# Kernel tuning notes

Hardware: AMD Instinct MI355X
Metric: run time of the kernel (lower is better)

Reference implementation:

```python
import jax, jax.numpy as jnp
import numpy as np

N_NODES = 50000


def gcn_conv(x, W, b, src, dst, n_nodes):
    # GCNConv (PyG defaults): h = x @ W; symmetric normalization with self-loops;
    # out[i] = sum_{(j->i) in E} d_j^-1/2 d_i^-1/2 h[j] + d_i^-1 h[i] + b
    h = x @ W
    ones = jnp.ones(src.shape[0], dtype=x.dtype)
    deg = jax.ops.segment_sum(ones, dst, num_segments=n_nodes) + 1.0  # +1 self-loop
    dinv = jax.lax.rsqrt(deg)
    norm = dinv[src] * dinv[dst]                       # [E]
    msg = h[src] * norm[:, None]                        # [E, D] gather
    agg = jax.ops.segment_sum(msg, dst, num_segments=n_nodes)  # scatter-add
    agg = agg + h * (dinv * dinv)[:, None]              # self-loop term
    return agg + b


def setup_inputs() -> dict:
    key = jax.random.key(0)
    k = jax.random.split(key, 8)
    in_dim, hid, out_dim = 128, 128, 64
    x = jax.random.normal(k[0], (N_NODES, in_dim), dtype=jnp.float32)
    edge_index = jax.random.randint(k[1], (2, 600000), 0, N_NODES, dtype=jnp.int64)
    s = 1.0 / np.sqrt(in_dim)
    W1 = jax.random.uniform(k[2], (in_dim, hid), jnp.float32, -s, s)
    b1 = jnp.zeros((hid,), jnp.float32)
    W2 = jax.random.uniform(k[3], (hid, hid), jnp.float32, -s, s)
    b2 = jnp.zeros((hid,), jnp.float32)
    W3 = jax.random.uniform(k[4], (hid, out_dim), jnp.float32, -s, s)
    b3 = jnp.zeros((out_dim,), jnp.float32)
    return {"x": x, "W1": W1, "b1": b1, "W2": W2, "b2": b2,
            "W3": W3, "b3": b3, "edge_index": edge_index}


def reference(x, W1, b1, W2, b2, W3, b3, edge_index):
    src, dst = edge_index[0], edge_index[1]
    n = x.shape[0]
    h = gcn_conv(x, W1, b1, src, dst, n)
    h = jax.nn.relu(h)  # dropout: inference-mode identity
    h = gcn_conv(h, W2, b2, src, dst, n)
    h = jax.nn.relu(h)
    h = gcn_conv(h, W3, b3, src, dst, n)
    return jax.nn.log_softmax(h, axis=-1)
```

## Files before the change

### kernel.cpp

```cpp
#include <hip/hip_runtime.h>
#include <math.h>

#define N_IN  128
#define N_HID 128
#define N_OUT 64

typedef _Float16 f16x8 __attribute__((ext_vector_type(8)));
typedef _Float16 f16x4 __attribute__((ext_vector_type(4)));
typedef float f32x4 __attribute__((ext_vector_type(4)));

__global__ void k_hist(const int* __restrict__ dst, int E, int* __restrict__ cnt) {
  int i0 = (blockIdx.x * blockDim.x + threadIdx.x) * 4;
  int stride = gridDim.x * blockDim.x * 4;
  for (; i0 + 4 <= E; i0 += stride) {
    int4 d = *reinterpret_cast<const int4*>(&dst[i0]);
    atomicAdd(&cnt[d.x], 1);
    atomicAdd(&cnt[d.y], 1);
    atomicAdd(&cnt[d.z], 1);
    atomicAdd(&cnt[d.w], 1);
  }
  if (i0 < E)
    for (; i0 < E; ++i0) atomicAdd(&cnt[dst[i0]], 1);
}

#define SCHUNK 512
__global__ __launch_bounds__(SCHUNK) void k_scan_all(
    const int* __restrict__ cnt, int n, int E,
    int* __restrict__ rowptr, float* __restrict__ dinv) {
  __shared__ int sh[SCHUNK];
  int t = threadIdx.x;
  int base = blockIdx.x * SCHUNK;
  int pre = 0;
  for (int i = t; i < base; i += SCHUNK) pre += cnt[i];
  sh[t] = pre;
  __syncthreads();
  for (int o = SCHUNK / 2; o > 0; o >>= 1) {
    if (t < o) sh[t] += sh[t + o];
    __syncthreads();
  }
  int blockpre = sh[0];
  __syncthreads();
  int v = (base + t < n) ? cnt[base + t] : 0;
  sh[t] = v;
  __syncthreads();
  for (int o = 1; o < SCHUNK; o <<= 1) {
    int u = (t >= o) ? sh[t - o] : 0;
    __syncthreads();
    sh[t] += u;
    __syncthreads();
  }
  int i = base + t;
  if (i < n) {
    rowptr[i] = blockpre + sh[t] - v;
    dinv[i] = rsqrtf((float)v + 1.0f);
    if (i == n - 1) rowptr[n] = E;
  }
}

__device__ inline void pack_one(const float* __restrict__ W, _Float16* __restrict__ Wp,
                                int N, int K, int idx) {
  int l = idx & 63;
  int ts = idx >> 6;
  int KS = K / 32;
  int t = ts / KS, s = ts - t * KS;
  int col = t * 16 + (l & 15);
  int k0 = s * 32 + (l >> 4) * 8;
  f16x8 f;
#pragma unroll
  for (int j = 0; j < 8; ++j) f[j] = (_Float16)W[(size_t)(k0 + j) * N + col];
  *reinterpret_cast<f16x8*>(&Wp[(size_t)idx * 8]) = f;
}

__global__ void k_fill_pack(const int* __restrict__ src, const int* __restrict__ dst,
                            int E, const int* __restrict__ rowptr, int* __restrict__ cnt,
                            int* __restrict__ csr, int fb,
                            const float* __restrict__ W1, const float* __restrict__ W2,
                            const float* __restrict__ W3, _Float16* __restrict__ Wp1,
                            _Float16* __restrict__ Wp2, _Float16* __restrict__ Wp3) {
  if (blockIdx.x >= fb) {
    int idx = (int)(blockIdx.x - fb) * 256 + threadIdx.x;
    if (idx < 2048) pack_one(W1, Wp1, N_HID, N_IN, idx);
    else if (idx < 4096) pack_one(W2, Wp2, N_HID, N_HID, idx - 2048);
    else if (idx < 5120) pack_one(W3, Wp3, N_OUT, N_HID, idx - 4096);
    return;
  }
  int i0 = (blockIdx.x * 256 + threadIdx.x) * 4;
  int stride = fb * 256 * 4;
  for (; i0 + 4 <= E; i0 += stride) {
    int4 d = *reinterpret_cast<const int4*>(&dst[i0]);
    int4 sr = *reinterpret_cast<const int4*>(&src[i0]);
    csr[rowptr[d.x] + atomicSub(&cnt[d.x], 1) - 1] = sr.x;
    csr[rowptr[d.y] + atomicSub(&cnt[d.y], 1) - 1] = sr.y;
    csr[rowptr[d.z] + atomicSub(&cnt[d.z], 1) - 1] = sr.z;
    csr[rowptr[d.w] + atomicSub(&cnt[d.w], 1) - 1] = sr.w;
  }
  if (i0 < E && threadIdx.x == 0 && blockIdx.x == 0)
    for (int i = (E >> 2) << 2; i < E; ++i) {
      int d = dst[i];
      csr[rowptr[d] + atomicSub(&cnt[d], 1) - 1] = src[i];
    }
}

__global__ __launch_bounds__(256) void k_gemm1(
    const float* __restrict__ A, const _Float16* __restrict__ Wp,
    const float* __restrict__ dinv, _Float16* __restrict__ out, int M) {
  constexpr int N = N_HID, K = 128, KS = K / 32, NT = N / 16;
  int lane = threadIdx.x & 63;
  int wave = threadIdx.x >> 6;
  int rowbase = blockIdx.x * 64 + wave * 16;
  int arow = rowbase + (lane & 15);
  int arc = arow < M ? arow : M - 1;
  int k0 = (lane >> 4) * 8;

  f16x8 afrag[KS];
#pragma unroll
  for (int s = 0; s < KS; ++s) {
    float4 v0 = *reinterpret_cast<const float4*>(&A[(size_t)arc * K + s * 32 + k0]);
    float4 v1 = *reinterpret_cast<const float4*>(&A[(size_t)arc * K + s * 32 + k0 + 4]);
    f16x8 f;
    f[0] = (_Float16)v0.x; f[1] = (_Float16)v0.y;
    f[2] = (_Float16)v0.z; f[3] = (_Float16)v0.w;
    f[4] = (_Float16)v1.x; f[5] = (_Float16)v1.y;
    f[6] = (_Float16)v1.z; f[7] = (_Float16)v1.w;
    afrag[s] = f;
  }

  f32x4 acc[NT] = {};
#pragma unroll
  for (int t = 0; t < NT; ++t)
#pragma unroll
    for (int s = 0; s < KS; ++s) {
      f16x8 b = *reinterpret_cast<const f16x8*>(&Wp[((size_t)(t * KS + s) * 64 + lane) * 8]);
      acc[t] = __builtin_amdgcn_mfma_f32_16x16x32_f16(afrag[s], b, acc[t], 0, 0, 0);
    }

  int crow = (lane >> 4) * 4;
  int col = lane & 15;
#pragma unroll
  for (int r = 0; r < 4; ++r) {
    int grow = rowbase + crow + r;
    if (grow < M) {
      float dv = dinv[grow];
#pragma unroll
      for (int t = 0; t < NT; ++t)
        out[(size_t)grow * N + t * 16 + col] = (_Float16)(acc[t][r] * dv);
    }
  }
}

template <int NOUT>
__global__ __launch_bounds__(256) void k_agg_gemm(
    const _Float16* __restrict__ hs, const float* __restrict__ dinv,
    const int* __restrict__ rowptr, const int* __restrict__ csr,
    const float* __restrict__ bias, const _Float16* __restrict__ Wp,
    _Float16* __restrict__ out, int n, int E) {
  constexpr int D = 128, KS = 4, NT = NOUT / 16, TPW = NT / 4;
  __shared__ __align__(16) _Float16 sm[16][D + 8];
  int lane = threadIdx.x & 63, wave = threadIdx.x >> 6;
  int h = lane >> 5;
  int j = lane & 31;
  int nodebase = blockIdx.x * 16;
  int nA = nodebase + wave * 4 + 2 * h;
  int nB = nA + 1;
  int cA = min(nA, n - 1), cB = min(nB, n - 1);
  float wsA = nA < n ? 1.f : 0.f, wsB = nB < n ? 1.f : 0.f;
  int begA = rowptr[cA], endA = nA < n ? rowptr[cA + 1] : begA;
  int begB = rowptr[cB], endB = nB < n ? rowptr[cB + 1] : begB;

  float accA[4], accB[4];
  {
    f16x4 sA = *reinterpret_cast<const f16x4*>(&hs[(size_t)cA * D + 4 * j]);
    f16x4 sB = *reinterpret_cast<const f16x4*>(&hs[(size_t)cB * D + 4 * j]);
#pragma unroll
    for (int k = 0; k < 4; ++k) {
      accA[k] = wsA * (float)sA[k];
      accB[k] = wsB * (float)sB[k];
    }
  }

  int eA = begA, eB = begB;
  int ia[4], ib[4];
  float wa[4], wb[4];
  auto loadIdx = [&](int a0, int b0, int* iax, int* ibx, float* wax, float* wbx) {
#pragma unroll
    for (int u = 0; u < 4; ++u) {
      int pA = a0 + u, pB = b0 + u;
      wax[u] = pA < endA ? 1.f : 0.f;
      wbx[u] = pB < endB ? 1.f : 0.f;
      iax[u] = csr[min(pA, E - 1)];
      ibx[u] = csr[min(pB, E - 1)];
    }
  };
  bool any = (eA < endA) || (eB < endB);
  if (any) loadIdx(eA, eB, ia, ib, wa, wb);
  while (any) {
    f16x4 va[4], vb[4];
#pragma unroll
    for (int u = 0; u < 4; ++u) {
      va[u] = *reinterpret_cast<const f16x4*>(&hs[(size_t)ia[u] * D + 4 * j]);
      vb[u] = *reinterpret_cast<const f16x4*>(&hs[(size_t)ib[u] * D + 4 * j]);
    }
    int eA2 = eA + 4, eB2 = eB + 4;
    bool any2 = (eA2 < endA) || (eB2 < endB);
    int ia2[4], ib2[4];
    float wa2[4], wb2[4];
    if (any2) loadIdx(eA2, eB2, ia2, ib2, wa2, wb2);
#pragma unroll
    for (int u = 0; u < 4; ++u)
#pragma unroll
      for (int k = 0; k < 4; ++k) {
        accA[k] = fmaf(wa[u], (float)va[u][k], accA[k]);
        accB[k] = fmaf(wb[u], (float)vb[u][k], accB[k]);
      }
    eA = eA2; eB = eB2; any = any2;
#pragma unroll
    for (int u = 0; u < 4; ++u) {
      ia[u] = ia2[u]; ib[u] = ib2[u];
      wa[u] = wa2[u]; wb[u] = wb2[u];
    }
  }

  {
    float4 bv = *reinterpret_cast<const float4*>(&bias[4 * j]);
    const float* bp = reinterpret_cast<const float*>(&bv);
    float dvA = dinv[cA], dvB = dinv[cB];
    f16x4 pA, pB;
#pragma unroll
    for (int k = 0; k < 4; ++k) {
      pA[k] = (_Float16)fmaxf(dvA * accA[k] + bp[k], 0.f);
      pB[k] = (_Float16)fmaxf(dvB * accB[k] + bp[k], 0.f);
    }
    int lr = wave * 4 + 2 * h;
    *reinterpret_cast<f16x4*>(&sm[lr][4 * j]) = pA;
    *reinterpret_cast<f16x4*>(&sm[lr + 1][4 * j]) = pB;
  }
  __syncthreads();

  int r = lane & 15, k0 = (lane >> 4) * 8;
  f16x8 af[KS];
#pragma unroll
  for (int s = 0; s < KS; ++s)
    af[s] = *reinterpret_cast<const f16x8*>(&sm[r][s * 32 + k0]);

  f32x4 acc[TPW] = {};
#pragma unroll
  for (int tt = 0; tt < TPW; ++tt) {
    int t = wave * TPW + tt;
#pragma unroll
    for (int s = 0; s < KS; ++s) {
      f16x8 b = *reinterpret_cast<const f16x8*>(&Wp[((size_t)(t * KS + s) * 64 + lane) * 8]);
      acc[tt] = __builtin_amdgcn_mfma_f32_16x16x32_f16(af[s], b, acc[tt], 0, 0, 0);
    }
  }

  int crow = (lane >> 4) * 4, col = lane & 15;
#pragma unroll
  for (int r4 = 0; r4 < 4; ++r4) {
    int node = nodebase + crow + r4;
    if (node < n) {
      float dv = dinv[node];
#pragma unroll
      for (int tt = 0; tt < TPW; ++tt)
        out[(size_t)node * NOUT + (wave * TPW + tt) * 16 + col] =
            (_Float16)(acc[tt][r4] * dv);
    }
  }
}

__global__ __launch_bounds__(256) void k_agg64_lsm(
    const _Float16* __restrict__ hs, const float* __restrict__ dinv,
    const int* __restrict__ rowptr, const int* __restrict__ csr,
    const float* __restrict__ bias, float* __restrict__ out, int n, int E) {
  constexpr int D = 64;
  int lane = threadIdx.x & 63, wave = threadIdx.x >> 6;
  int q = lane >> 4, j = lane & 15;
  int node = blockIdx.x * 16 + wave * 4 + q;
  int c = min(node, n - 1);
  float ws = node < n ? 1.f : 0.f;
  int beg = rowptr[c], end = node < n ? rowptr[c + 1] : beg;

  float acc[4];
  {
    f16x4 sv = *reinterpret_cast<const f16x4*>(&hs[(size_t)c * D + 4 * j]);
#pragma unroll
    for (int k = 0; k < 4; ++k) acc[k] = ws * (float)sv[k];
  }

  int e = beg;
  int ii[4];
  float ww[4];
  auto loadIdx = [&](int e0, int* iix, float* wwx) {
#pragma unroll
    for (int u = 0; u < 4; ++u) {
      int p = e0 + u;
      wwx[u] = p < end ? 1.f : 0.f;
      iix[u] = csr[min(p, E - 1)];
    }
  };
  bool any = e < end;
  if (any) loadIdx(e, ii, ww);
  while (any) {
    f16x4 vv[4];
#pragma unroll
    for (int u = 0; u < 4; ++u)
      vv[u] = *reinterpret_cast<const f16x4*>(&hs[(size_t)ii[u] * D + 4 * j]);
    int e2 = e + 4;
    bool any2 = e2 < end;
    int ii2[4];
    float ww2[4];
    if (any2) loadIdx(e2, ii2, ww2);
#pragma unroll
    for (int u = 0; u < 4; ++u)
#pragma unroll
      for (int k = 0; k < 4; ++k) acc[k] = fmaf(ww[u], (float)vv[u][k], acc[k]);
    e = e2; any = any2;
#pragma unroll
    for (int u = 0; u < 4; ++u) { ii[u] = ii2[u]; ww[u] = ww2[u]; }
  }

  float dv = dinv[c];
  float val[4];
#pragma unroll
  for (int k = 0; k < 4; ++k) val[k] = dv * acc[k] + bias[4 * j + k];

  float m = fmaxf(fmaxf(val[0], val[1]), fmaxf(val[2], val[3]));
#pragma unroll
  for (int o = 8; o > 0; o >>= 1) m = fmaxf(m, __shfl_xor(m, o));
  float ss = 0.f;
#pragma unroll
  for (int k = 0; k < 4; ++k) ss += expf(val[k] - m);
#pragma unroll
  for (int o = 8; o > 0; o >>= 1) ss += __shfl_xor(ss, o);
  float lse = m + logf(ss);

  if (node < n) {
    float4 o4 = make_float4(val[0] - lse, val[1] - lse, val[2] - lse, val[3] - lse);
    *reinterpret_cast<float4*>(&out[(size_t)node * D + 4 * j]) = o4;
  }
}

extern "C" void kernel_launch(void* const* d_in, const int* in_sizes, int n_in,
                              void* d_out, int out_size, void* d_ws, size_t ws_size,
                              hipStream_t stream) {
  const float* x  = (const float*)d_in[0];
  const float* W1 = (const float*)d_in[1];
  const float* b1 = (const float*)d_in[2];
  const float* W2 = (const float*)d_in[3];
  const float* b2 = (const float*)d_in[4];
  const float* W3 = (const float*)d_in[5];
  const float* b3 = (const float*)d_in[6];
  const int*   ei = (const int*)d_in[7];

  int n = in_sizes[0] / N_IN;
  int E = in_sizes[7] / 2;
  const int* src = ei;
  const int* dst = ei + E;

  char* w = (char*)d_ws;
  size_t off = 0;
  auto alloc = [&](size_t bytes) -> void* {
    void* p = w + off;
    off = (off + bytes + 255) & ~(size_t)255;
    return p;
  };
  _Float16* hs1 = (_Float16*)alloc((size_t)n * N_HID * sizeof(_Float16));
  _Float16* hs2 = (_Float16*)alloc((size_t)n * N_HID * sizeof(_Float16));
  _Float16* hs3 = (_Float16*)alloc((size_t)n * N_OUT * sizeof(_Float16));
  _Float16* Wp1 = (_Float16*)alloc((size_t)N_IN * N_HID * sizeof(_Float16));
  _Float16* Wp2 = (_Float16*)alloc((size_t)N_HID * N_HID * sizeof(_Float16));
  _Float16* Wp3 = (_Float16*)alloc((size_t)N_HID * N_OUT * sizeof(_Float16));
  float* dinv = (float*)alloc((size_t)n * sizeof(float));
  int* cnt = (int*)alloc((size_t)n * sizeof(int));
  int* rowptr = (int*)alloc((size_t)(n + 1) * sizeof(int));
  int* csr = (int*)alloc((size_t)E * sizeof(int));

  hipMemsetAsync(cnt, 0, (size_t)n * sizeof(int), stream);
  int fb = min((E / 4 + 255) / 256, 1024);
  k_hist<<<fb, 256, 0, stream>>>(dst, E, cnt);
  int nb = (n + SCHUNK - 1) / SCHUNK;
  k_scan_all<<<nb, SCHUNK, 0, stream>>>(cnt, n, E, rowptr, dinv);
  k_fill_pack<<<fb + 20, 256, 0, stream>>>(src, dst, E, rowptr, cnt, csr, fb,
                                           W1, W2, W3, Wp1, Wp2, Wp3);

  int gb = (n + 63) / 64;
  int ab = (n + 15) / 16;
  k_gemm1<<<gb, 256, 0, stream>>>(x, Wp1, dinv, hs1, n);
  k_agg_gemm<N_HID><<<ab, 256, 0, stream>>>(hs1, dinv, rowptr, csr, b1, Wp2, hs2, n, E);
  k_agg_gemm<N_OUT><<<ab, 256, 0, stream>>>(hs2, dinv, rowptr, csr, b2, Wp3, hs3, n, E);
  k_agg64_lsm<<<ab, 256, 0, stream>>>(hs3, dinv, rowptr, csr, b3, (float*)d_out, n, E);
}
```

Measured before the change: 176.1 us.

## Fuse weight packing into histogram, gemm1 into CSR fill, widen aggregation gathers

```diff
diff --git a/kernel.cpp b/kernel.cpp
--- a/kernel.cpp
+++ b/kernel.cpp
@@ -9,9 +9,34 @@
 typedef _Float16 f16x4 __attribute__((ext_vector_type(4)));
 typedef float f32x4 __attribute__((ext_vector_type(4)));
 
-__global__ void k_hist(const int* __restrict__ dst, int E, int* __restrict__ cnt) {
-  int i0 = (blockIdx.x * blockDim.x + threadIdx.x) * 4;
-  int stride = gridDim.x * blockDim.x * 4;
+__device__ inline void pack_one(const float* __restrict__ W, _Float16* __restrict__ Wp,
+                                int N, int K, int idx) {
+  int l = idx & 63;
+  int ts = idx >> 6;
+  int KS = K / 32;
+  int t = ts / KS, s = ts - t * KS;
+  int col = t * 16 + (l & 15);
+  int k0 = s * 32 + (l >> 4) * 8;
+  f16x8 f;
+#pragma unroll
+  for (int j = 0; j < 8; ++j) f[j] = (_Float16)W[(size_t)(k0 + j) * N + col];
+  *reinterpret_cast<f16x8*>(&Wp[(size_t)idx * 8]) = f;
+}
+
+__global__ void k_hist_pack(const int* __restrict__ dst, int E, int* __restrict__ cnt,
+                            int hb,
+                            const float* __restrict__ W1, const float* __restrict__ W2,
+                            const float* __restrict__ W3, _Float16* __restrict__ Wp1,
+                            _Float16* __restrict__ Wp2, _Float16* __restrict__ Wp3) {
+  if (blockIdx.x >= hb) {
+    int idx = (int)(blockIdx.x - hb) * 256 + threadIdx.x;
+    if (idx < 2048) pack_one(W1, Wp1, N_HID, N_IN, idx);
+    else if (idx < 4096) pack_one(W2, Wp2, N_HID, N_HID, idx - 2048);
+    else if (idx < 5120) pack_one(W3, Wp3, N_OUT, N_HID, idx - 4096);
+    return;
+  }
+  int i0 = (blockIdx.x * 256 + threadIdx.x) * 4;
+  int stride = hb * 256 * 4;
   for (; i0 + 4 <= E; i0 += stride) {
     int4 d = *reinterpret_cast<const int4*>(&dst[i0]);
     atomicAdd(&cnt[d.x], 1);
@@ -19,8 +44,8 @@
     atomicAdd(&cnt[d.z], 1);
     atomicAdd(&cnt[d.w], 1);
   }
-  if (i0 < E)
-    for (; i0 < E; ++i0) atomicAdd(&cnt[dst[i0]], 1);
+  if (blockIdx.x == 0 && threadIdx.x == 0)
+    for (int i = E & ~3; i < E; ++i) atomicAdd(&cnt[dst[i]], 1);
 }
 
 #define SCHUNK 512
@@ -57,31 +82,61 @@
   }
 }
 
-__device__ inline void pack_one(const float* __restrict__ W, _Float16* __restrict__ Wp,
-                                int N, int K, int idx) {
-  int l = idx & 63;
-  int ts = idx >> 6;
-  int KS = K / 32;
-  int t = ts / KS, s = ts - t * KS;
-  int col = t * 16 + (l & 15);
-  int k0 = s * 32 + (l >> 4) * 8;
-  f16x8 f;
-#pragma unroll
-  for (int j = 0; j < 8; ++j) f[j] = (_Float16)W[(size_t)(k0 + j) * N + col];
-  *reinterpret_cast<f16x8*>(&Wp[(size_t)idx * 8]) = f;
-}
-
-__global__ void k_fill_pack(const int* __restrict__ src, const int* __restrict__ dst,
-                            int E, const int* __restrict__ rowptr, int* __restrict__ cnt,
-                            int* __restrict__ csr, int fb,
-                            const float* __restrict__ W1, const float* __restrict__ W2,
-                            const float* __restrict__ W3, _Float16* __restrict__ Wp1,
-                            _Float16* __restrict__ Wp2, _Float16* __restrict__ Wp3) {
+__device__ inline void gemm1_body(int bid, const float* __restrict__ A,
+                                  const _Float16* __restrict__ Wp,
+                                  const float* __restrict__ dinv,
+                                  _Float16* __restrict__ out, int M) {
+  constexpr int N = N_HID, K = 128, KS = K / 32, NT = N / 16;
+  int lane = threadIdx.x & 63;
+  int wave = threadIdx.x >> 6;
+  int rowbase = bid * 64 + wave * 16;
+  int arow = rowbase + (lane & 15);
+  int arc = arow < M ? arow : M - 1;
+  int k0 = (lane >> 4) * 8;
+
+  f16x8 afrag[KS];
+#pragma unroll
+  for (int s = 0; s < KS; ++s) {
+    float4 v0 = *reinterpret_cast<const float4*>(&A[(size_t)arc * K + s * 32 + k0]);
+    float4 v1 = *reinterpret_cast<const float4*>(&A[(size_t)arc * K + s * 32 + k0 + 4]);
+    f16x8 f;
+    f[0] = (_Float16)v0.x; f[1] = (_Float16)v0.y;
+    f[2] = (_Float16)v0.z; f[3] = (_Float16)v0.w;
+    f[4] = (_Float16)v1.x; f[5] = (_Float16)v1.y;
+    f[6] = (_Float16)v1.z; f[7] = (_Float16)v1.w;
+    afrag[s] = f;
+  }
+
+  f32x4 acc[NT] = {};
+#pragma unroll
+  for (int t = 0; t < NT; ++t)
+#pragma unroll
+    for (int s = 0; s < KS; ++s) {
+      f16x8 b = *reinterpret_cast<const f16x8*>(&Wp[((size_t)(t * KS + s) * 64 + lane) * 8]);
+      acc[t] = __builtin_amdgcn_mfma_f32_16x16x32_f16(afrag[s], b, acc[t], 0, 0, 0);
+    }
+
+  int crow = (lane >> 4) * 4;
+  int col = lane & 15;
+#pragma unroll
+  for (int r = 0; r < 4; ++r) {
+    int grow = rowbase + crow + r;
+    if (grow < M) {
+      float dv = dinv[grow];
+#pragma unroll
+      for (int t = 0; t < NT; ++t)
+        out[(size_t)grow * N + t * 16 + col] = (_Float16)(acc[t][r] * dv);
+    }
+  }
+}
+
+__global__ __launch_bounds__(256) void k_fill_gemm1(
+    const int* __restrict__ src, const int* __restrict__ dst, int E,
+    const int* __restrict__ rowptr, int* __restrict__ cnt, int* __restrict__ csr,
+    int fb, const float* __restrict__ x, const _Float16* __restrict__ Wp1,
+    const float* __restrict__ dinv, _Float16* __restrict__ hs1, int n) {
   if (blockIdx.x >= fb) {
-    int idx = (int)(blockIdx.x - fb) * 256 + threadIdx.x;
-    if (idx < 2048) pack_one(W1, Wp1, N_HID, N_IN, idx);
-    else if (idx < 4096) pack_one(W2, Wp2, N_HID, N_HID, idx - 2048);
-    else if (idx < 5120) pack_one(W3, Wp3, N_OUT, N_HID, idx - 4096);
+    gemm1_body((int)blockIdx.x - fb, x, Wp1, dinv, hs1, n);
     return;
   }
   int i0 = (blockIdx.x * 256 + threadIdx.x) * 4;
@@ -94,58 +149,11 @@
     csr[rowptr[d.z] + atomicSub(&cnt[d.z], 1) - 1] = sr.z;
     csr[rowptr[d.w] + atomicSub(&cnt[d.w], 1) - 1] = sr.w;
   }
-  if (i0 < E && threadIdx.x == 0 && blockIdx.x == 0)
-    for (int i = (E >> 2) << 2; i < E; ++i) {
+  if (blockIdx.x == 0 && threadIdx.x == 0)
+    for (int i = E & ~3; i < E; ++i) {
       int d = dst[i];
       csr[rowptr[d] + atomicSub(&cnt[d], 1) - 1] = src[i];
     }
-}
-
-__global__ __launch_bounds__(256) void k_gemm1(
-    const float* __restrict__ A, const _Float16* __restrict__ Wp,
-    const float* __restrict__ dinv, _Float16* __restrict__ out, int M) {
-  constexpr int N = N_HID, K = 128, KS = K / 32, NT = N / 16;
-  int lane = threadIdx.x & 63;
-  int wave = threadIdx.x >> 6;
-  int rowbase = blockIdx.x * 64 + wave * 16;
-  int arow = rowbase + (lane & 15);
-  int arc = arow < M ? arow : M - 1;
-  int k0 = (lane >> 4) * 8;
-
-  f16x8 afrag[KS];
-#pragma unroll
-  for (int s = 0; s < KS; ++s) {
-    float4 v0 = *reinterpret_cast<const float4*>(&A[(size_t)arc * K + s * 32 + k0]);
-    float4 v1 = *reinterpret_cast<const float4*>(&A[(size_t)arc * K + s * 32 + k0 + 4]);
-    f16x8 f;
-    f[0] = (_Float16)v0.x; f[1] = (_Float16)v0.y;
-    f[2] = (_Float16)v0.z; f[3] = (_Float16)v0.w;
-    f[4] = (_Float16)v1.x; f[5] = (_Float16)v1.y;
-    f[6] = (_Float16)v1.z; f[7] = (_Float16)v1.w;
-    afrag[s] = f;
-  }
-
-  f32x4 acc[NT] = {};
-#pragma unroll
-  for (int t = 0; t < NT; ++t)
-#pragma unroll
-    for (int s = 0; s < KS; ++s) {
-      f16x8 b = *reinterpret_cast<const f16x8*>(&Wp[((size_t)(t * KS + s) * 64 + lane) * 8]);
-      acc[t] = __builtin_amdgcn_mfma_f32_16x16x32_f16(afrag[s], b, acc[t], 0, 0, 0);
-    }
-
-  int crow = (lane >> 4) * 4;
-  int col = lane & 15;
-#pragma unroll
-  for (int r = 0; r < 4; ++r) {
-    int grow = rowbase + crow + r;
-    if (grow < M) {
-      float dv = dinv[grow];
-#pragma unroll
-      for (int t = 0; t < NT; ++t)
-        out[(size_t)grow * N + t * 16 + col] = (_Float16)(acc[t][r] * dv);
-    }
-  }
 }
 
 template <int NOUT>
@@ -157,82 +165,50 @@
   constexpr int D = 128, KS = 4, NT = NOUT / 16, TPW = NT / 4;
   __shared__ __align__(16) _Float16 sm[16][D + 8];
   int lane = threadIdx.x & 63, wave = threadIdx.x >> 6;
-  int h = lane >> 5;
-  int j = lane & 31;
+  int q = lane >> 4;
+  int j = lane & 15;
   int nodebase = blockIdx.x * 16;
-  int nA = nodebase + wave * 4 + 2 * h;
-  int nB = nA + 1;
-  int cA = min(nA, n - 1), cB = min(nB, n - 1);
-  float wsA = nA < n ? 1.f : 0.f, wsB = nB < n ? 1.f : 0.f;
-  int begA = rowptr[cA], endA = nA < n ? rowptr[cA + 1] : begA;
-  int begB = rowptr[cB], endB = nB < n ? rowptr[cB + 1] : begB;
-
-  float accA[4], accB[4];
+  int node = nodebase + wave * 4 + q;
+  int cn = min(node, n - 1);
+  bool valid = node < n;
+  int beg = rowptr[cn], end = valid ? rowptr[cn + 1] : beg;
+
+  float acc[8];
   {
-    f16x4 sA = *reinterpret_cast<const f16x4*>(&hs[(size_t)cA * D + 4 * j]);
-    f16x4 sB = *reinterpret_cast<const f16x4*>(&hs[(size_t)cB * D + 4 * j]);
-#pragma unroll
-    for (int k = 0; k < 4; ++k) {
-      accA[k] = wsA * (float)sA[k];
-      accB[k] = wsB * (float)sB[k];
-    }
-  }
-
-  int eA = begA, eB = begB;
-  int ia[4], ib[4];
-  float wa[4], wb[4];
-  auto loadIdx = [&](int a0, int b0, int* iax, int* ibx, float* wax, float* wbx) {
+    f16x8 sv = *reinterpret_cast<const f16x8*>(&hs[(size_t)cn * D + 8 * j]);
+#pragma unroll
+    for (int k = 0; k < 8; ++k) acc[k] = valid ? (float)sv[k] : 0.f;
+  }
+
+  for (int e = beg; e < end; e += 4) {
+    int idx[4];
+    float wt[4];
 #pragma unroll
     for (int u = 0; u < 4; ++u) {
-      int pA = a0 + u, pB = b0 + u;
-      wax[u] = pA < endA ? 1.f : 0.f;
-      wbx[u] = pB < endB ? 1.f : 0.f;
-      iax[u] = csr[min(pA, E - 1)];
-      ibx[u] = csr[min(pB, E - 1)];
-    }
-  };
-  bool any = (eA < endA) || (eB < endB);
-  if (any) loadIdx(eA, eB, ia, ib, wa, wb);
-  while (any) {
-    f16x4 va[4], vb[4];
-#pragma unroll
-    for (int u = 0; u < 4; ++u) {
-      va[u] = *reinterpret_cast<const f16x4*>(&hs[(size_t)ia[u] * D + 4 * j]);
-      vb[u] = *reinterpret_cast<const f16x4*>(&hs[(size_t)ib[u] * D + 4 * j]);
-    }
-    int eA2 = eA + 4, eB2 = eB + 4;
-    bool any2 = (eA2 < endA) || (eB2 < endB);
-    int ia2[4], ib2[4];
-    float wa2[4], wb2[4];
-    if (any2) loadIdx(eA2, eB2, ia2, ib2, wa2, wb2);
+      int p = e + u;
+      wt[u] = p < end ? 1.f : 0.f;
+      idx[u] = csr[min(p, E - 1)];
+    }
+    f16x8 v[4];
 #pragma unroll
     for (int u = 0; u < 4; ++u)
-#pragma unroll
-      for (int k = 0; k < 4; ++k) {
-        accA[k] = fmaf(wa[u], (float)va[u][k], accA[k]);
-        accB[k] = fmaf(wb[u], (float)vb[u][k], accB[k]);
-      }
-    eA = eA2; eB = eB2; any = any2;
-#pragma unroll
-    for (int u = 0; u < 4; ++u) {
-      ia[u] = ia2[u]; ib[u] = ib2[u];
-      wa[u] = wa2[u]; wb[u] = wb2[u];
-    }
+      v[u] = *reinterpret_cast<const f16x8*>(&hs[(size_t)idx[u] * D + 8 * j]);
+#pragma unroll
+    for (int u = 0; u < 4; ++u)
+#pragma unroll
+      for (int k = 0; k < 8; ++k)
+        acc[k] = fmaf(wt[u], (float)v[u][k], acc[k]);
   }
 
   {
-    float4 bv = *reinterpret_cast<const float4*>(&bias[4 * j]);
-    const float* bp = reinterpret_cast<const float*>(&bv);
-    float dvA = dinv[cA], dvB = dinv[cB];
-    f16x4 pA, pB;
-#pragma unroll
-    for (int k = 0; k < 4; ++k) {
-      pA[k] = (_Float16)fmaxf(dvA * accA[k] + bp[k], 0.f);
-      pB[k] = (_Float16)fmaxf(dvB * accB[k] + bp[k], 0.f);
-    }
-    int lr = wave * 4 + 2 * h;
-    *reinterpret_cast<f16x4*>(&sm[lr][4 * j]) = pA;
-    *reinterpret_cast<f16x4*>(&sm[lr + 1][4 * j]) = pB;
+    float4 bv0 = *reinterpret_cast<const float4*>(&bias[8 * j]);
+    float4 bv1 = *reinterpret_cast<const float4*>(&bias[8 * j + 4]);
+    float bp[8] = {bv0.x, bv0.y, bv0.z, bv0.w, bv1.x, bv1.y, bv1.z, bv1.w};
+    float dv = dinv[cn];
+    f16x8 pv;
+#pragma unroll
+    for (int k = 0; k < 8; ++k) pv[k] = (_Float16)fmaxf(dv * acc[k] + bp[k], 0.f);
+    *reinterpret_cast<f16x8*>(&sm[wave * 4 + q][8 * j]) = pv;
   }
   __syncthreads();
 
@@ -242,27 +218,27 @@
   for (int s = 0; s < KS; ++s)
     af[s] = *reinterpret_cast<const f16x8*>(&sm[r][s * 32 + k0]);
 
-  f32x4 acc[TPW] = {};
+  f32x4 acc2[TPW] = {};
 #pragma unroll
   for (int tt = 0; tt < TPW; ++tt) {
     int t = wave * TPW + tt;
 #pragma unroll
     for (int s = 0; s < KS; ++s) {
       f16x8 b = *reinterpret_cast<const f16x8*>(&Wp[((size_t)(t * KS + s) * 64 + lane) * 8]);
-      acc[tt] = __builtin_amdgcn_mfma_f32_16x16x32_f16(af[s], b, acc[tt], 0, 0, 0);
+      acc2[tt] = __builtin_amdgcn_mfma_f32_16x16x32_f16(af[s], b, acc2[tt], 0, 0, 0);
     }
   }
 
   int crow = (lane >> 4) * 4, col = lane & 15;
 #pragma unroll
   for (int r4 = 0; r4 < 4; ++r4) {
-    int node = nodebase + crow + r4;
-    if (node < n) {
-      float dv = dinv[node];
+    int gnode = nodebase + crow + r4;
+    if (gnode < n) {
+      float dv = dinv[gnode];
 #pragma unroll
       for (int tt = 0; tt < TPW; ++tt)
-        out[(size_t)node * NOUT + (wave * TPW + tt) * 16 + col] =
-            (_Float16)(acc[tt][r4] * dv);
+        out[(size_t)gnode * NOUT + (wave * TPW + tt) * 16 + col] =
+            (_Float16)(acc2[tt][r4] * dv);
     }
   }
 }
@@ -273,69 +249,67 @@
     const float* __restrict__ bias, float* __restrict__ out, int n, int E) {
   constexpr int D = 64;
   int lane = threadIdx.x & 63, wave = threadIdx.x >> 6;
-  int q = lane >> 4, j = lane & 15;
-  int node = blockIdx.x * 16 + wave * 4 + q;
-  int c = min(node, n - 1);
-  float ws = node < n ? 1.f : 0.f;
-  int beg = rowptr[c], end = node < n ? rowptr[c + 1] : beg;
-
-  float acc[4];
+  int g = lane >> 3;
+  int j = lane & 7;
+  int node = blockIdx.x * 32 + wave * 8 + g;
+  int cn = min(node, n - 1);
+  bool valid = node < n;
+  int beg = rowptr[cn], end = valid ? rowptr[cn + 1] : beg;
+
+  float acc[8];
   {
-    f16x4 sv = *reinterpret_cast<const f16x4*>(&hs[(size_t)c * D + 4 * j]);
-#pragma unroll
-    for (int k = 0; k < 4; ++k) acc[k] = ws * (float)sv[k];
-  }
-
-  int e = beg;
-  int ii[4];
-  float ww[4];
-  auto loadIdx = [&](int e0, int* iix, float* wwx) {
+    f16x8 sv = *reinterpret_cast<const f16x8*>(&hs[(size_t)cn * D + 8 * j]);
+#pragma unroll
+    for (int k = 0; k < 8; ++k) acc[k] = valid ? (float)sv[k] : 0.f;
+  }
+
+  for (int e = beg; e < end; e += 4) {
+    int idx[4];
+    float wt[4];
 #pragma unroll
     for (int u = 0; u < 4; ++u) {
-      int p = e0 + u;
-      wwx[u] = p < end ? 1.f : 0.f;
-      iix[u] = csr[min(p, E - 1)];
-    }
-  };
-  bool any = e < end;
-  if (any) loadIdx(e, ii, ww);
-  while (any) {
-    f16x4 vv[4];
+      int p = e + u;
+      wt[u] = p < end ? 1.f : 0.f;
+      idx[u] = csr[min(p, E - 1)];
+    }
+    f16x8 v[4];
 #pragma unroll
     for (int u = 0; u < 4; ++u)
-      vv[u] = *reinterpret_cast<const f16x4*>(&hs[(size_t)ii[u] * D + 4 * j]);
-    int e2 = e + 4;
-    bool any2 = e2 < end;
-    int ii2[4];
-    float ww2[4];
-    if (any2) loadIdx(e2, ii2, ww2);
+      v[u] = *reinterpret_cast<const f16x8*>(&hs[(size_t)idx[u] * D + 8 * j]);
 #pragma unroll
     for (int u = 0; u < 4; ++u)
 #pragma unroll
-      for (int k = 0; k < 4; ++k) acc[k] = fmaf(ww[u], (float)vv[u][k], acc[k]);
-    e = e2; any = any2;
-#pragma unroll
-    for (int u = 0; u < 4; ++u) { ii[u] = ii2[u]; ww[u] = ww2[u]; }
-  }
-
-  float dv = dinv[c];
-  float val[4];
-#pragma unroll
-  for (int k = 0; k < 4; ++k) val[k] = dv * acc[k] + bias[4 * j + k];
-
-  float m = fmaxf(fmaxf(val[0], val[1]), fmaxf(val[2], val[3]));
-#pragma unroll
-  for (int o = 8; o > 0; o >>= 1) m = fmaxf(m, __shfl_xor(m, o));
+      for (int k = 0; k < 8; ++k)
+        acc[k] = fmaf(wt[u], (float)v[u][k], acc[k]);
+  }
+
+  float dv = dinv[cn];
+  float val[8];
+  {
+    float4 bv0 = *reinterpret_cast<const float4*>(&bias[8 * j]);
+    float4 bv1 = *reinterpret_cast<const float4*>(&bias[8 * j + 4]);
+    float bp[8] = {bv0.x, bv0.y, bv0.z, bv0.w, bv1.x, bv1.y, bv1.z, bv1.w};
+#pragma unroll
+    for (int k = 0; k < 8; ++k) val[k] = dv * acc[k] + bp[k];
+  }
+
+  float m = val[0];
+#pragma unroll
+  for (int k = 1; k < 8; ++k) m = fmaxf(m, val[k]);
+#pragma unroll
+  for (int o = 4; o > 0; o >>= 1) m = fmaxf(m, __shfl_xor(m, o));
   float ss = 0.f;
 #pragma unroll
-  for (int k = 0; k < 4; ++k) ss += expf(val[k] - m);
-#pragma unroll
-  for (int o = 8; o > 0; o >>= 1) ss += __shfl_xor(ss, o);
+  for (int k = 0; k < 8; ++k) ss += expf(val[k] - m);
+#pragma unroll
+  for (int o = 4; o > 0; o >>= 1) ss += __shfl_xor(ss, o);
   float lse = m + logf(ss);
 
-  if (node < n) {
-    float4 o4 = make_float4(val[0] - lse, val[1] - lse, val[2] - lse, val[3] - lse);
-    *reinterpret_cast<float4*>(&out[(size_t)node * D + 4 * j]) = o4;
+  if (valid) {
+    float4 o0 = make_float4(val[0] - lse, val[1] - lse, val[2] - lse, val[3] - lse);
+    float4 o1 = make_float4(val[4] - lse, val[5] - lse, val[6] - lse, val[7] - lse);
+    *reinterpret_cast<float4*>(&out[(size_t)node * D + 8 * j]) = o0;
+    *reinterpret_cast<float4*>(&out[(size_t)node * D + 8 * j + 4]) = o1;
   }
 }
 
@@ -375,17 +349,17 @@
   int* csr = (int*)alloc((size_t)E * sizeof(int));
 
   hipMemsetAsync(cnt, 0, (size_t)n * sizeof(int), stream);
-  int fb = min((E / 4 + 255) / 256, 1024);
-  k_hist<<<fb, 256, 0, stream>>>(dst, E, cnt);
+  int hb = min((E / 4 + 255) / 256, 1024);
+  k_hist_pack<<<hb + 20, 256, 0, stream>>>(dst, E, cnt, hb, W1, W2, W3, Wp1, Wp2, Wp3);
   int nb = (n + SCHUNK - 1) / SCHUNK;
   k_scan_all<<<nb, SCHUNK, 0, stream>>>(cnt, n, E, rowptr, dinv);
-  k_fill_pack<<<fb + 20, 256, 0, stream>>>(src, dst, E, rowptr, cnt, csr, fb,
-                                           W1, W2, W3, Wp1, Wp2, Wp3);
-
   int gb = (n + 63) / 64;
+  k_fill_gemm1<<<hb + gb, 256, 0, stream>>>(src, dst, E, rowptr, cnt, csr, hb,
+                                            x, Wp1, dinv, hs1, n);
+
   int ab = (n + 15) / 16;
-  k_gemm1<<<gb, 256, 0, stream>>>(x, Wp1, dinv, hs1, n);
+  int ab64 = (n + 31) / 32;
   k_agg_gemm<N_HID><<<ab, 256, 0, stream>>>(hs1, dinv, rowptr, csr, b1, Wp2, hs2, n, E);
   k_agg_gemm<N_OUT><<<ab, 256, 0, stream>>>(hs2, dinv, rowptr, csr, b2, Wp3, hs3, n, E);
-  k_agg64_lsm<<<ab, 256, 0, stream>>>(hs3, dinv, rowptr, csr, b3, (float*)d_out, n, E);
-}
+  k_agg64_lsm<<<ab64, 256, 0, stream>>>(hs3, dinv, rowptr, csr, b3, (float*)d_out, n, E);
+}
```

New measurement: 164.4 us. -6.7%, faster.
